# Kernel optimization log

Measured on AMD Instinct MI355X. Metric: run time of the kernel, lower is better.

## Reference

```python
import jax, jax.numpy as jnp
import numpy as np

H = 30  # hidden size
D_IN = 4
D_OUT = 4


def setup_inputs() -> dict:
    key = jax.random.key(0)
    ks = jax.random.split(key, 12)
    s = 0.1
    inp = {
        "input": jax.random.normal(ks[0], (2048, 1024, D_IN), dtype=jnp.float32),
        "W_ih1": jax.random.normal(ks[1], (4 * H, D_IN), dtype=jnp.float32) * s,
        "b_ih1": jax.random.normal(ks[2], (4 * H,), dtype=jnp.float32) * s,
        "W_hh1": jax.random.normal(ks[3], (4 * H, H), dtype=jnp.float32) * s,
        "b_hh1": jax.random.normal(ks[4], (4 * H,), dtype=jnp.float32) * s,
        "W_ih2": jax.random.normal(ks[5], (4 * H, H), dtype=jnp.float32) * s,
        "b_ih2": jax.random.normal(ks[6], (4 * H,), dtype=jnp.float32) * s,
        "W_hh2": jax.random.normal(ks[7], (4 * H, H), dtype=jnp.float32) * s,
        "b_hh2": jax.random.normal(ks[8], (4 * H,), dtype=jnp.float32) * s,
        "W_lin": jax.random.normal(ks[9], (D_OUT, H), dtype=jnp.float32) * s,
        "b_lin": jax.random.normal(ks[10], (D_OUT,), dtype=jnp.float32) * s,
        "future": 0,
    }
    return inp


def _lstm_cell(x, h, c, W_ih, b_ih, W_hh, b_hh):
    # PyTorch LSTMCell gate order: i, f, g, o
    gates = x @ W_ih.T + b_ih + h @ W_hh.T + b_hh  # [B, 4H]
    i, f, g, o = jnp.split(gates, 4, axis=-1)
    i = jax.nn.sigmoid(i)
    f = jax.nn.sigmoid(f)
    g = jnp.tanh(g)
    o = jax.nn.sigmoid(o)
    c_new = f * c + i * g
    h_new = o * jnp.tanh(c_new)
    return h_new, c_new


def reference(input, W_ih1, b_ih1, W_hh1, b_hh1, W_ih2, b_ih2, W_hh2, b_hh2,
              W_lin, b_lin, future):
    B, T, _ = input.shape

    def step(carry, x_t):
        h1, c1, h2, c2 = carry
        h1, c1 = _lstm_cell(x_t[:, :D_IN], h1, c1, W_ih1, b_ih1, W_hh1, b_hh1)
        h2, c2 = _lstm_cell(h1, h2, c2, W_ih2, b_ih2, W_hh2, b_hh2)
        out = h2 @ W_lin.T + b_lin  # [B, 4]
        return (h1, c1, h2, c2), out

    z = jnp.zeros((B, H), dtype=input.dtype)
    carry0 = (z, z, z, z)
    carry, outs = jax.lax.scan(step, carry0, jnp.transpose(input, (1, 0, 2)))
    outputs = jnp.transpose(outs, (1, 0, 2))  # [B, T, 4]

    if future > 0:
        h1, c1, h2, c2 = carry
        out = outputs[:, -1, :]
        fut = []
        for _ in range(future):
            h1, c1 = _lstm_cell(out, h1, c1, W_ih1, b_ih1, W_hh1, b_hh1)
            h2, c2 = _lstm_cell(h1, h2, c2, W_ih2, b_ih2, W_hh2, b_hh2)
            out = h2 @ W_lin.T + b_lin
            fut.append(out)
        outputs = jnp.concatenate([outputs, jnp.stack(fut, axis=1)], axis=1)
    return outputs
```

## Files before the change

kernel.cpp:

```cpp
#include <hip/hip_runtime.h>

typedef float f32x4 __attribute__((ext_vector_type(4)));
typedef float v4f  __attribute__((ext_vector_type(4)));
typedef _Float16 half8 __attribute__((ext_vector_type(8)));
typedef unsigned int u32;
typedef unsigned short u16;

#define HH 30
#define DIN 4
#define DOUT 4
#define NB 16
#define L2E 1.44269504088896340736f

#if __has_builtin(__builtin_amdgcn_exp2f)
#define EXP2F(v) __builtin_amdgcn_exp2f(v)
#else
#define EXP2F(v) exp2f(v)
#endif

__device__ __forceinline__ float sig2f(float v) {
    return __builtin_amdgcn_rcpf(1.0f + EXP2F(v));
}

__device__ __forceinline__ f32x4 MF(half8 a, half8 b, f32x4 c) {
    return __builtin_amdgcn_mfma_f32_16x16x32_f16(a, b, c, 0, 0, 0);
}

union F8 { half8 h; _Float16 e[8]; u32 w[4]; };
union HU { _Float16 h; u16 s; };

__device__ __forceinline__ void lds_barrier() {
    __builtin_amdgcn_sched_barrier(0);
    asm volatile("s_waitcnt lgkmcnt(0)" ::: "memory");
    __builtin_amdgcn_sched_barrier(0);
    __builtin_amdgcn_s_barrier();
    __builtin_amdgcn_sched_barrier(0);
}

__global__ __launch_bounds__(256)
void lstm2_kernel(const float* __restrict__ x,
                  const float* __restrict__ Wih1, const float* __restrict__ bih1,
                  const float* __restrict__ Whh1, const float* __restrict__ bhh1,
                  const float* __restrict__ Wih2, const float* __restrict__ bih2,
                  const float* __restrict__ Whh2, const float* __restrict__ bhh2,
                  const float* __restrict__ Wlin, const float* __restrict__ blin,
                  float* __restrict__ out, int T)
{
    const int tid = threadIdx.x;
    const int w = tid >> 6;
    const int l = tid & 63;
    const int n = l & 15;
    const int p = l >> 4;
    const int b0 = blockIdx.x * NB;
    const float M2 = -2.0f * L2E;

    __shared__ __align__(16) u16 lds[2][4][16][40];

    {
        u32* z = reinterpret_cast<u32*>(&lds[0][0][0][0]);
        const int tot = 2 * 4 * 16 * 40 / 2;
        for (int i = tid; i < tot; i += 256) z[i] = 0u;
    }

    const int gA = n & 3;
    const float scA = (gA == 2) ? -2.0f * L2E : -L2E;

    half8 a1h_h[2], a1h_l[2];
    half8 a1x_h[2], a1x_l[2];
    half8 a2i_h[2], a2i_l[2];
    half8 a2h_h[2], a2h_l[2];
    f32x4 bias1f[2], bias2f[2];

#pragma unroll
    for (int ri = 0; ri < 2; ++ri) {
        const int rt = 2 * w + ri;
        const int qA = 4 * rt + (n >> 2);
        F8 Hh, Hl, Xh, Xl, Ih, Il, Rh, Rl;
#pragma unroll
        for (int e = 0; e < 8; ++e) {
            const int k = 16 * (e >> 2) + 4 * p + (e & 3);
            float v; _Float16 t16;
            v = (qA < HH && k < HH) ? Whh1[(gA * HH + qA) * HH + k] * scA : 0.0f;
            t16 = (_Float16)v; Hh.e[e] = t16; Hl.e[e] = (_Float16)(v - (float)t16);
            v = (qA < HH && k < DIN) ? Wih1[(gA * HH + qA) * DIN + k] * scA : 0.0f;
            t16 = (_Float16)v; Xh.e[e] = t16; Xl.e[e] = (_Float16)(v - (float)t16);
            v = (qA < HH && k < HH) ? Wih2[(gA * HH + qA) * HH + k] * scA : 0.0f;
            t16 = (_Float16)v; Ih.e[e] = t16; Il.e[e] = (_Float16)(v - (float)t16);
            v = (qA < HH && k < HH) ? Whh2[(gA * HH + qA) * HH + k] * scA : 0.0f;
            t16 = (_Float16)v; Rh.e[e] = t16; Rl.e[e] = (_Float16)(v - (float)t16);
        }
        a1h_h[ri] = Hh.h; a1h_l[ri] = Hl.h;
        a1x_h[ri] = Xh.h; a1x_l[ri] = Xl.h;
        a2i_h[ri] = Ih.h; a2i_l[ri] = Il.h;
        a2h_h[ri] = Rh.h; a2h_l[ri] = Rl.h;

        const int qC = 4 * rt + p;
        f32x4 b1, b2;
#pragma unroll
        for (int r = 0; r < 4; ++r) {
            const float scr = (r == 2) ? -2.0f * L2E : -L2E;
            b1[r] = (qC < HH) ? (bih1[r * HH + qC] + bhh1[r * HH + qC]) * scr : 0.0f;
            b2[r] = (qC < HH) ? (bih2[r * HH + qC] + bhh2[r * HH + qC]) * scr : 0.0f;
        }
        bias1f[ri] = b1; bias2f[ri] = b2;
    }

    half8 alin_h, alin_l;
    f32x4 blinf;
    {
        F8 Lh, Ll;
#pragma unroll
        for (int e = 0; e < 8; ++e) {
            const int k = 16 * (e >> 2) + 4 * p + (e & 3);
            float v = (n < DOUT && k < HH) ? Wlin[n * HH + k] : 0.0f;
            _Float16 t16 = (_Float16)v;
            Lh.e[e] = t16; Ll.e[e] = (_Float16)(v - (float)t16);
        }
        alin_h = Lh.h; alin_l = Ll.h;
#pragma unroll
        for (int r = 0; r < 4; ++r)
            blinf[r] = (p == 0) ? blin[r] : 0.0f;
    }

    float c1[2] = {0.0f, 0.0f}, c2[2] = {0.0f, 0.0f};
    half8 bh1_h, bh1_l, bh2_h, bh2_l;

    const v4f* xp = reinterpret_cast<const v4f*>(x) + (size_t)(b0 + n) * T;
    v4f xc = xp[0];

    __syncthreads();

    {
        F8 XH, XL;
#pragma unroll
        for (int e = 0; e < 8; ++e) { XH.e[e] = (_Float16)0.0f; XL.e[e] = (_Float16)0.0f; }
        if (p == 0) {
#pragma unroll
            for (int e = 0; e < 4; ++e) {
                _Float16 t16 = (_Float16)xc[e];
                XH.e[e] = t16; XL.e[e] = (_Float16)(xc[e] - (float)t16);
            }
        }
        const half8 bx_h = XH.h, bx_l = XL.h;
#pragma unroll
        for (int ri = 0; ri < 2; ++ri) {
            f32x4 g1 = bias1f[ri];
            g1 = MF(a1x_h[ri], bx_h, g1);
            g1 = MF(a1x_h[ri], bx_l, g1);
            g1 = MF(a1x_l[ri], bx_h, g1);
            const float iv = sig2f(g1[0]);
            const float fv = sig2f(g1[1]);
            const float gg = fmaf(2.0f, sig2f(g1[2]), -1.0f);
            const float ov = sig2f(g1[3]);
            c1[ri] = fmaf(fv, c1[ri], iv * gg);
            const float h1n = ov * fmaf(2.0f, sig2f(M2 * c1[ri]), -1.0f);
            const int kq = 8 * w + 4 * ri + p;
            const int pos = ((kq & 15) >> 2) * 8 + (kq >> 4) * 4 + (kq & 3);
            HU hi, lo;
            hi.h = (_Float16)h1n;
            lo.h = (_Float16)(h1n - (float)hi.h);
            lds[0][0][n][pos] = (kq < HH) ? hi.s : (u16)0;
            lds[0][1][n][pos] = (kq < HH) ? lo.s : (u16)0;
        }
    }
    __syncthreads();
    {
        bh1_h = *reinterpret_cast<const half8*>(&lds[0][0][n][8 * p]);
        bh1_l = *reinterpret_cast<const half8*>(&lds[0][1][n][8 * p]);
        bh2_h = *reinterpret_cast<const half8*>(&lds[0][2][n][8 * p]);
        bh2_l = *reinterpret_cast<const half8*>(&lds[0][3][n][8 * p]);
    }
    xc = xp[(T > 1) ? 1 : 0];

    const f32x4 zf = {0.0f, 0.0f, 0.0f, 0.0f};

    for (int t = 0; t < T; ++t) {
        F8 XH, XL;
#pragma unroll
        for (int e = 0; e < 8; ++e) { XH.e[e] = (_Float16)0.0f; XL.e[e] = (_Float16)0.0f; }
        if (p == 0) {
#pragma unroll
            for (int e = 0; e < 4; ++e) {
                _Float16 t16 = (_Float16)xc[e];
                XH.e[e] = t16; XL.e[e] = (_Float16)(xc[e] - (float)t16);
            }
        }
        const half8 bx_h = XH.h, bx_l = XL.h;

        const int bw = (t + 1) & 1;
#pragma unroll
        for (int ri = 0; ri < 2; ++ri) {
            f32x4 g2a = bias2f[ri];
            g2a = MF(a2i_h[ri], bh1_h, g2a);
            g2a = MF(a2i_h[ri], bh1_l, g2a);
            g2a = MF(a2i_l[ri], bh1_h, g2a);
            f32x4 g2b = zf;
            g2b = MF(a2h_h[ri], bh2_h, g2b);
            g2b = MF(a2h_h[ri], bh2_l, g2b);
            g2b = MF(a2h_l[ri], bh2_h, g2b);
            const f32x4 g2 = g2a + g2b;
            f32x4 g1a = bias1f[ri];
            g1a = MF(a1h_h[ri], bh1_h, g1a);
            g1a = MF(a1h_h[ri], bh1_l, g1a);
            g1a = MF(a1h_l[ri], bh1_h, g1a);
            f32x4 g1b = zf;
            g1b = MF(a1x_h[ri], bx_h, g1b);
            g1b = MF(a1x_h[ri], bx_l, g1b);
            g1b = MF(a1x_l[ri], bx_h, g1b);
            const f32x4 g1 = g1a + g1b;

            const float iv2 = sig2f(g2[0]);
            const float fv2 = sig2f(g2[1]);
            const float gg2 = fmaf(2.0f, sig2f(g2[2]), -1.0f);
            const float ov2 = sig2f(g2[3]);
            c2[ri] = fmaf(fv2, c2[ri], iv2 * gg2);
            const float h2n = ov2 * fmaf(2.0f, sig2f(M2 * c2[ri]), -1.0f);

            const float iv1 = sig2f(g1[0]);
            const float fv1 = sig2f(g1[1]);
            const float gg1 = fmaf(2.0f, sig2f(g1[2]), -1.0f);
            const float ov1 = sig2f(g1[3]);
            c1[ri] = fmaf(fv1, c1[ri], iv1 * gg1);
            const float h1n = ov1 * fmaf(2.0f, sig2f(M2 * c1[ri]), -1.0f);

            const int kq = 8 * w + 4 * ri + p;
            const int pos = ((kq & 15) >> 2) * 8 + (kq >> 4) * 4 + (kq & 3);
            HU h1hi, h1lo, h2hi, h2lo;
            h1hi.h = (_Float16)h1n;
            h1lo.h = (_Float16)(h1n - (float)h1hi.h);
            h2hi.h = (_Float16)h2n;
            h2lo.h = (_Float16)(h2n - (float)h2hi.h);
            const bool ok = (kq < HH);
            lds[bw][0][n][pos] = ok ? h1hi.s : (u16)0;
            lds[bw][1][n][pos] = ok ? h1lo.s : (u16)0;
            lds[bw][2][n][pos] = ok ? h2hi.s : (u16)0;
            lds[bw][3][n][pos] = ok ? h2lo.s : (u16)0;
        }

        lds_barrier();

        bh1_h = *reinterpret_cast<const half8*>(&lds[bw][0][n][8 * p]);
        bh1_l = *reinterpret_cast<const half8*>(&lds[bw][1][n][8 * p]);
        bh2_h = *reinterpret_cast<const half8*>(&lds[bw][2][n][8 * p]);
        bh2_l = *reinterpret_cast<const half8*>(&lds[bw][3][n][8 * p]);

        const v4f xn = xp[(t + 2 < T) ? (t + 2) : (T - 1)];

        if (w == 3) {
            f32x4 oh = blinf;
            oh = MF(alin_h, bh2_h, oh);
            oh = MF(alin_h, bh2_l, oh);
            oh = MF(alin_l, bh2_h, oh);
            if (p == 0) {
                v4f ov;
                ov.x = oh[0]; ov.y = oh[1]; ov.z = oh[2]; ov.w = oh[3];
                *reinterpret_cast<v4f*>(out + (((size_t)(b0 + n)) * T + t) * DOUT) = ov;
            }
        }
        xc = xn;
    }
}

extern "C" void kernel_launch(void* const* d_in, const int* in_sizes, int n_in,
                              void* d_out, int out_size, void* d_ws, size_t ws_size,
                              hipStream_t stream)
{
    const float* x    = (const float*)d_in[0];
    const float* Wih1 = (const float*)d_in[1];
    const float* bih1 = (const float*)d_in[2];
    const float* Whh1 = (const float*)d_in[3];
    const float* bhh1 = (const float*)d_in[4];
    const float* Wih2 = (const float*)d_in[5];
    const float* bih2 = (const float*)d_in[6];
    const float* Whh2 = (const float*)d_in[7];
    const float* bhh2 = (const float*)d_in[8];
    const float* Wlin = (const float*)d_in[9];
    const float* blin = (const float*)d_in[10];
    float* out = (float*)d_out;

    const int T = 1024;
    const int B = in_sizes[0] / (T * DIN);

    hipLaunchKernelGGL(lstm2_kernel, dim3(B / NB), dim3(256), 0, stream,
                       x, Wih1, bih1, Whh1, bhh1, Wih2, bih2, Whh2, bhh2,
                       Wlin, blin, out, T);
}
```

Before: 917.0 us.

## Spread hidden-unit row tiles across 8 waves instead of 4

Doubles the block to 512 threads so each wave owns one 4-unit row tile instead of two, halving per-wave MFMA and activation work on the serial time-step chain. The input fp16 split conversion moves out of the loop head into the post-barrier section, with the x prefetch pushed one step further ahead. This adds more waves to each barrier and may reduce occupancy per CU with a grid of only 128 blocks.

```diff
diff --git a/kernel.cpp b/kernel.cpp
--- a/kernel.cpp
+++ b/kernel.cpp
@@ -37,7 +37,7 @@
     __builtin_amdgcn_sched_barrier(0);
 }
 
-__global__ __launch_bounds__(256)
+__global__ __launch_bounds__(512)
 void lstm2_kernel(const float* __restrict__ x,
                   const float* __restrict__ Wih1, const float* __restrict__ bih1,
                   const float* __restrict__ Whh1, const float* __restrict__ bhh1,
@@ -59,22 +59,18 @@
     {
         u32* z = reinterpret_cast<u32*>(&lds[0][0][0][0]);
         const int tot = 2 * 4 * 16 * 40 / 2;
-        for (int i = tid; i < tot; i += 256) z[i] = 0u;
+        for (int i = tid; i < tot; i += 512) z[i] = 0u;
     }
 
     const int gA = n & 3;
     const float scA = (gA == 2) ? -2.0f * L2E : -L2E;
-
-    half8 a1h_h[2], a1h_l[2];
-    half8 a1x_h[2], a1x_l[2];
-    half8 a2i_h[2], a2i_l[2];
-    half8 a2h_h[2], a2h_l[2];
-    f32x4 bias1f[2], bias2f[2];
-
-#pragma unroll
-    for (int ri = 0; ri < 2; ++ri) {
-        const int rt = 2 * w + ri;
-        const int qA = 4 * rt + (n >> 2);
+    const int qA = 4 * w + (n >> 2);
+
+    half8 a1h_h, a1h_l;
+    half8 a1x_h, a1x_l;
+    half8 a2i_h, a2i_l;
+    half8 a2h_h, a2h_l;
+    {
         F8 Hh, Hl, Xh, Xl, Ih, Il, Rh, Rl;
 #pragma unroll
         for (int e = 0; e < 8; ++e) {
@@ -89,20 +85,22 @@
             v = (qA < HH && k < HH) ? Whh2[(gA * HH + qA) * HH + k] * scA : 0.0f;
             t16 = (_Float16)v; Rh.e[e] = t16; Rl.e[e] = (_Float16)(v - (float)t16);
         }
-        a1h_h[ri] = Hh.h; a1h_l[ri] = Hl.h;
-        a1x_h[ri] = Xh.h; a1x_l[ri] = Xl.h;
-        a2i_h[ri] = Ih.h; a2i_l[ri] = Il.h;
-        a2h_h[ri] = Rh.h; a2h_l[ri] = Rl.h;
-
-        const int qC = 4 * rt + p;
-        f32x4 b1, b2;
-#pragma unroll
-        for (int r = 0; r < 4; ++r) {
-            const float scr = (r == 2) ? -2.0f * L2E : -L2E;
-            b1[r] = (qC < HH) ? (bih1[r * HH + qC] + bhh1[r * HH + qC]) * scr : 0.0f;
-            b2[r] = (qC < HH) ? (bih2[r * HH + qC] + bhh2[r * HH + qC]) * scr : 0.0f;
-        }
-        bias1f[ri] = b1; bias2f[ri] = b2;
+        a1h_h = Hh.h; a1h_l = Hl.h;
+        a1x_h = Xh.h; a1x_l = Xl.h;
+        a2i_h = Ih.h; a2i_l = Il.h;
+        a2h_h = Rh.h; a2h_l = Rl.h;
+    }
+
+    const int kq = 4 * w + p;
+    const bool okq = (kq < HH);
+    const int pos = ((kq & 15) >> 2) * 8 + (kq >> 4) * 4 + (kq & 3);
+
+    f32x4 bias1f, bias2f;
+#pragma unroll
+    for (int r = 0; r < 4; ++r) {
+        const float scr = (r == 2) ? -2.0f * L2E : -L2E;
+        bias1f[r] = okq ? (bih1[r * HH + kq] + bhh1[r * HH + kq]) * scr : 0.0f;
+        bias2f[r] = okq ? (bih2[r * HH + kq] + bhh2[r * HH + kq]) * scr : 0.0f;
     }
 
     half8 alin_h, alin_l;
@@ -122,11 +120,11 @@
             blinf[r] = (p == 0) ? blin[r] : 0.0f;
     }
 
-    float c1[2] = {0.0f, 0.0f}, c2[2] = {0.0f, 0.0f};
+    float c1 = 0.0f, c2 = 0.0f;
     half8 bh1_h, bh1_l, bh2_h, bh2_l;
 
     const v4f* xp = reinterpret_cast<const v4f*>(x) + (size_t)(b0 + n) * T;
-    v4f xc = xp[0];
+    const v4f x0 = xp[0];
 
     __syncthreads();
 
@@ -137,105 +135,95 @@
         if (p == 0) {
 #pragma unroll
             for (int e = 0; e < 4; ++e) {
-                _Float16 t16 = (_Float16)xc[e];
-                XH.e[e] = t16; XL.e[e] = (_Float16)(xc[e] - (float)t16);
-            }
-        }
-        const half8 bx_h = XH.h, bx_l = XL.h;
-#pragma unroll
-        for (int ri = 0; ri < 2; ++ri) {
-            f32x4 g1 = bias1f[ri];
-            g1 = MF(a1x_h[ri], bx_h, g1);
-            g1 = MF(a1x_h[ri], bx_l, g1);
-            g1 = MF(a1x_l[ri], bx_h, g1);
-            const float iv = sig2f(g1[0]);
-            const float fv = sig2f(g1[1]);
-            const float gg = fmaf(2.0f, sig2f(g1[2]), -1.0f);
-            const float ov = sig2f(g1[3]);
-            c1[ri] = fmaf(fv, c1[ri], iv * gg);
-            const float h1n = ov * fmaf(2.0f, sig2f(M2 * c1[ri]), -1.0f);
-            const int kq = 8 * w + 4 * ri + p;
-            const int pos = ((kq & 15) >> 2) * 8 + (kq >> 4) * 4 + (kq & 3);
-            HU hi, lo;
-            hi.h = (_Float16)h1n;
-            lo.h = (_Float16)(h1n - (float)hi.h);
-            lds[0][0][n][pos] = (kq < HH) ? hi.s : (u16)0;
-            lds[0][1][n][pos] = (kq < HH) ? lo.s : (u16)0;
-        }
+                _Float16 t16 = (_Float16)x0[e];
+                XH.e[e] = t16; XL.e[e] = (_Float16)(x0[e] - (float)t16);
+            }
+        }
+        f32x4 g1 = bias1f;
+        g1 = MF(a1x_h, XH.h, g1);
+        g1 = MF(a1x_h, XL.h, g1);
+        g1 = MF(a1x_l, XH.h, g1);
+        const float iv = sig2f(g1[0]);
+        const float fv = sig2f(g1[1]);
+        const float gg = fmaf(2.0f, sig2f(g1[2]), -1.0f);
+        const float ov = sig2f(g1[3]);
+        c1 = fmaf(fv, c1, iv * gg);
+        const float h1n = ov * fmaf(2.0f, sig2f(M2 * c1), -1.0f);
+        HU hi, lo;
+        hi.h = (_Float16)h1n;
+        lo.h = (_Float16)(h1n - (float)hi.h);
+        lds[0][0][n][pos] = okq ? hi.s : (u16)0;
+        lds[0][1][n][pos] = okq ? lo.s : (u16)0;
     }
     __syncthreads();
-    {
-        bh1_h = *reinterpret_cast<const half8*>(&lds[0][0][n][8 * p]);
-        bh1_l = *reinterpret_cast<const half8*>(&lds[0][1][n][8 * p]);
-        bh2_h = *reinterpret_cast<const half8*>(&lds[0][2][n][8 * p]);
-        bh2_l = *reinterpret_cast<const half8*>(&lds[0][3][n][8 * p]);
-    }
-    xc = xp[(T > 1) ? 1 : 0];
-
-    const f32x4 zf = {0.0f, 0.0f, 0.0f, 0.0f};
-
-    for (int t = 0; t < T; ++t) {
+    bh1_h = *reinterpret_cast<const half8*>(&lds[0][0][n][8 * p]);
+    bh1_l = *reinterpret_cast<const half8*>(&lds[0][1][n][8 * p]);
+    bh2_h = *reinterpret_cast<const half8*>(&lds[0][2][n][8 * p]);
+    bh2_l = *reinterpret_cast<const half8*>(&lds[0][3][n][8 * p]);
+
+    half8 bx_h, bx_l;
+    {
+        const v4f x1 = xp[(T > 1) ? 1 : 0];
         F8 XH, XL;
 #pragma unroll
         for (int e = 0; e < 8; ++e) { XH.e[e] = (_Float16)0.0f; XL.e[e] = (_Float16)0.0f; }
         if (p == 0) {
 #pragma unroll
             for (int e = 0; e < 4; ++e) {
-                _Float16 t16 = (_Float16)xc[e];
-                XH.e[e] = t16; XL.e[e] = (_Float16)(xc[e] - (float)t16);
-            }
-        }
-        const half8 bx_h = XH.h, bx_l = XL.h;
+                _Float16 t16 = (_Float16)x1[e];
+                XH.e[e] = t16; XL.e[e] = (_Float16)(x1[e] - (float)t16);
+            }
+        }
+        bx_h = XH.h; bx_l = XL.h;
+    }
+    v4f xn = xp[(T > 2) ? 2 : (T - 1)];
+
+    const f32x4 zf = {0.0f, 0.0f, 0.0f, 0.0f};
+
+    for (int t = 0; t < T; ++t) {
+        f32x4 g2a = bias2f;
+        g2a = MF(a2i_h, bh1_h, g2a);
+        g2a = MF(a2i_h, bh1_l, g2a);
+        g2a = MF(a2i_l, bh1_h, g2a);
+        f32x4 g2b = zf;
+        g2b = MF(a2h_h, bh2_h, g2b);
+        g2b = MF(a2h_h, bh2_l, g2b);
+        g2b = MF(a2h_l, bh2_h, g2b);
+        const f32x4 g2 = g2a + g2b;
+        f32x4 g1a = bias1f;
+        g1a = MF(a1h_h, bh1_h, g1a);
+        g1a = MF(a1h_h, bh1_l, g1a);
+        g1a = MF(a1h_l, bh1_h, g1a);
+        f32x4 g1b = zf;
+        g1b = MF(a1x_h, bx_h, g1b);
+        g1b = MF(a1x_h, bx_l, g1b);
+        g1b = MF(a1x_l, bx_h, g1b);
+        const f32x4 g1 = g1a + g1b;
+
+        const float iv2 = sig2f(g2[0]);
+        const float fv2 = sig2f(g2[1]);
+        const float gg2 = fmaf(2.0f, sig2f(g2[2]), -1.0f);
+        const float ov2 = sig2f(g2[3]);
+        c2 = fmaf(fv2, c2, iv2 * gg2);
+        const float h2n = ov2 * fmaf(2.0f, sig2f(M2 * c2), -1.0f);
+
+        const float iv1 = sig2f(g1[0]);
+        const float fv1 = sig2f(g1[1]);
+        const float gg1 = fmaf(2.0f, sig2f(g1[2]), -1.0f);
+        const float ov1 = sig2f(g1[3]);
+        c1 = fmaf(fv1, c1, iv1 * gg1);
+        const float h1n = ov1 * fmaf(2.0f, sig2f(M2 * c1), -1.0f);
 
         const int bw = (t + 1) & 1;
-#pragma unroll
-        for (int ri = 0; ri < 2; ++ri) {
-            f32x4 g2a = bias2f[ri];
-            g2a = MF(a2i_h[ri], bh1_h, g2a);
-            g2a = MF(a2i_h[ri], bh1_l, g2a);
-            g2a = MF(a2i_l[ri], bh1_h, g2a);
-            f32x4 g2b = zf;
-            g2b = MF(a2h_h[ri], bh2_h, g2b);
-            g2b = MF(a2h_h[ri], bh2_l, g2b);
-            g2b = MF(a2h_l[ri], bh2_h, g2b);
-            const f32x4 g2 = g2a + g2b;
-            f32x4 g1a = bias1f[ri];
-            g1a = MF(a1h_h[ri], bh1_h, g1a);
-            g1a = MF(a1h_h[ri], bh1_l, g1a);
-            g1a = MF(a1h_l[ri], bh1_h, g1a);
-            f32x4 g1b = zf;
-            g1b = MF(a1x_h[ri], bx_h, g1b);
-            g1b = MF(a1x_h[ri], bx_l, g1b);
-            g1b = MF(a1x_l[ri], bx_h, g1b);
-            const f32x4 g1 = g1a + g1b;
-
-            const float iv2 = sig2f(g2[0]);
-            const float fv2 = sig2f(g2[1]);
-            const float gg2 = fmaf(2.0f, sig2f(g2[2]), -1.0f);
-            const float ov2 = sig2f(g2[3]);
-            c2[ri] = fmaf(fv2, c2[ri], iv2 * gg2);
-            const float h2n = ov2 * fmaf(2.0f, sig2f(M2 * c2[ri]), -1.0f);
-
-            const float iv1 = sig2f(g1[0]);
-            const float fv1 = sig2f(g1[1]);
-            const float gg1 = fmaf(2.0f, sig2f(g1[2]), -1.0f);
-            const float ov1 = sig2f(g1[3]);
-            c1[ri] = fmaf(fv1, c1[ri], iv1 * gg1);
-            const float h1n = ov1 * fmaf(2.0f, sig2f(M2 * c1[ri]), -1.0f);
-
-            const int kq = 8 * w + 4 * ri + p;
-            const int pos = ((kq & 15) >> 2) * 8 + (kq >> 4) * 4 + (kq & 3);
-            HU h1hi, h1lo, h2hi, h2lo;
-            h1hi.h = (_Float16)h1n;
-            h1lo.h = (_Float16)(h1n - (float)h1hi.h);
-            h2hi.h = (_Float16)h2n;
-            h2lo.h = (_Float16)(h2n - (float)h2hi.h);
-            const bool ok = (kq < HH);
-            lds[bw][0][n][pos] = ok ? h1hi.s : (u16)0;
-            lds[bw][1][n][pos] = ok ? h1lo.s : (u16)0;
-            lds[bw][2][n][pos] = ok ? h2hi.s : (u16)0;
-            lds[bw][3][n][pos] = ok ? h2lo.s : (u16)0;
-        }
+        HU h1hi, h1lo, h2hi, h2lo;
+        h1hi.h = (_Float16)h1n;
+        h1lo.h = (_Float16)(h1n - (float)h1hi.h);
+        h2hi.h = (_Float16)h2n;
+        h2lo.h = (_Float16)(h2n - (float)h2hi.h);
+        lds[bw][0][n][pos] = okq ? h1hi.s : (u16)0;
+        lds[bw][1][n][pos] = okq ? h1lo.s : (u16)0;
+        lds[bw][2][n][pos] = okq ? h2hi.s : (u16)0;
+        lds[bw][3][n][pos] = okq ? h2lo.s : (u16)0;
 
         lds_barrier();
 
@@ -244,9 +232,22 @@
         bh2_h = *reinterpret_cast<const half8*>(&lds[bw][2][n][8 * p]);
         bh2_l = *reinterpret_cast<const half8*>(&lds[bw][3][n][8 * p]);
 
-        const v4f xn = xp[(t + 2 < T) ? (t + 2) : (T - 1)];
-
-        if (w == 3) {
+        {
+            F8 XH, XL;
+#pragma unroll
+            for (int e = 0; e < 8; ++e) { XH.e[e] = (_Float16)0.0f; XL.e[e] = (_Float16)0.0f; }
+            if (p == 0) {
+#pragma unroll
+                for (int e = 0; e < 4; ++e) {
+                    _Float16 t16 = (_Float16)xn[e];
+                    XH.e[e] = t16; XL.e[e] = (_Float16)(xn[e] - (float)t16);
+                }
+            }
+            bx_h = XH.h; bx_l = XL.h;
+        }
+        xn = xp[(t + 3 < T) ? (t + 3) : (T - 1)];
+
+        if (w == 7) {
             f32x4 oh = blinf;
             oh = MF(alin_h, bh2_h, oh);
             oh = MF(alin_h, bh2_l, oh);
@@ -257,7 +258,6 @@
                 *reinterpret_cast<v4f*>(out + (((size_t)(b0 + n)) * T + t) * DOUT) = ov;
             }
         }
-        xc = xn;
     }
 }
 
@@ -281,7 +281,7 @@
     const int T = 1024;
     const int B = in_sizes[0] / (T * DIN);
 
-    hipLaunchKernelGGL(lstm2_kernel, dim3(B / NB), dim3(256), 0, stream,
+    hipLaunchKernelGGL(lstm2_kernel, dim3(B / NB), dim3(512), 0, stream,
                        x, Wih1, bih1, Whh1, bhh1, Wih2, bih2, Whh2, bhh2,
                        Wlin, blin, out, T);
 }
```

Measured after the change: 762.0 us. 1.2x faster.
